# Performance work log

Hardware: AMD Instinct MI355X
Metric: run time of the kernel (lower is better)

## Reference

```python
import jax, jax.numpy as jnp
import numpy as np

B, S, D, H = 2, 2048, 2048, 16
HD = D // H


def setup_inputs() -> dict:
    key = jax.random.key(0)
    ks = jax.random.split(key, 9)
    scale = 0.02
    return {
        "x": jax.random.normal(ks[0], (B, S, D), dtype=jnp.float32),
        "wq_w": jax.random.normal(ks[1], (D, D), dtype=jnp.float32) * scale,
        "wq_b": jnp.zeros((D,), dtype=jnp.float32),
        "wk_w": jax.random.normal(ks[2], (D, D), dtype=jnp.float32) * scale,
        "wk_b": jnp.zeros((D,), dtype=jnp.float32),
        "wv_w": jax.random.normal(ks[3], (D, D), dtype=jnp.float32) * scale,
        "wv_b": jnp.zeros((D,), dtype=jnp.float32),
        "wo_w": jax.random.normal(ks[4], (D, D), dtype=jnp.float32) * scale,
        "wo_b": jnp.zeros((D,), dtype=jnp.float32),
    }


def reference(x, wq_w, wq_b, wk_w, wk_b, wv_w, wv_b, wo_w, wo_b):
    # torch Linear: y = x @ W.T + b
    q = x @ wq_w.T + wq_b  # [B,S,D]
    k = x @ wk_w.T + wk_b
    v = x @ wv_w.T + wv_b
    # [B,S,D] -> [B,H,S,HD]
    q = q.reshape(B, S, H, HD).transpose(0, 2, 1, 3)
    k = k.reshape(B, S, H, HD).transpose(0, 2, 1, 3)
    v = v.reshape(B, S, H, HD).transpose(0, 2, 1, 3)
    # scores [B,H,S,S], scaled by sqrt(d_dim) as in the original (not head_dim)
    scores = jnp.einsum("bhid,bhjd->bhij", q, k) / np.float32(np.sqrt(D))
    # faithful reproduction of the module's triu/transpose masking:
    m = jnp.swapaxes(jnp.triu(scores), -2, -1)  # lower-tri, zeros elsewhere
    p = jax.nn.softmax(m, axis=-2)              # softmax over dim=-2, zeros included
    a = jnp.swapaxes(jnp.triu(p), -2, -1)       # [B,H,S,S]
    attn = jnp.einsum("bhij,bhjd->bhid", a, v)  # [B,H,S,HD]
    concat = attn.transpose(0, 2, 1, 3).reshape(B, S, D)
    return concat @ wo_w.T + wo_b
```

## Files before the change

kernel.cpp:

```cpp
#include <hip/hip_runtime.h>

#define BB 2
#define SS 2048
#define DD 2048
#define HH 16
#define HDIM 128
#define MTOK (BB*SS)
#define BHH (BB*HH)
#define NCHUNK 16
#define QKN (2*DD)

typedef __attribute__((ext_vector_type(8))) __bf16 bf16x8;
typedef __attribute__((ext_vector_type(4))) float f32x4;
typedef __attribute__((ext_vector_type(8))) int i32x8;
typedef __attribute__((ext_vector_type(4))) int i32x4;

__device__ __forceinline__ unsigned short f2bf(float f) {
  unsigned u = __float_as_uint(f);
  u += 0x7FFFu + ((u >> 16) & 1u);
  return (unsigned short)(u >> 16);
}
__device__ __forceinline__ float bf2f(unsigned short s) {
  return __uint_as_float(((unsigned)s) << 16);
}
__device__ __forceinline__ unsigned char f2e4m3(float f) {
  int pk = __builtin_amdgcn_cvt_pk_fp8_f32(f, f, 0, false);
  return (unsigned char)(pk & 0xFF);
}

#define GLOAD_LDS16(src, dst)                                                   \
  __builtin_amdgcn_global_load_lds(                                             \
      (const void __attribute__((address_space(1)))*)(src),                     \
      (void __attribute__((address_space(3)))*)(dst), 16, 0, 0)

__device__ __forceinline__ void barrier_raw() {
  asm volatile("" ::: "memory");
  __builtin_amdgcn_s_barrier();
  asm volatile("" ::: "memory");
}

__global__ void cvt_x_dual(const float* __restrict__ in,
                           unsigned short* __restrict__ outb,
                           unsigned int* __restrict__ out8, int n4) {
  int i = blockIdx.x * blockDim.x + threadIdx.x;
  if (i < n4) {
    float4 v = ((const float4*)in)[i];
    ushort4 o;
    o.x = f2bf(v.x); o.y = f2bf(v.y); o.z = f2bf(v.z); o.w = f2bf(v.w);
    ((ushort4*)outb)[i] = o;
    int p0 = __builtin_amdgcn_cvt_pk_fp8_f32(v.x, v.y, 0, false);
    int p1 = __builtin_amdgcn_cvt_pk_fp8_f32(v.z, v.w, 0, false);
    out8[i] = (unsigned)(p0 & 0xFFFF) | ((unsigned)(p1 & 0xFFFF) << 16);
  }
}

__global__ void cvt_wqk8(const float* __restrict__ a, const float* __restrict__ b,
                         unsigned int* __restrict__ out) {
  int i = blockIdx.x * blockDim.x + threadIdx.x;
  int sel = i >> 20, r = i & 0xFFFFF;
  const float* src = sel == 0 ? a : b;
  float4 v = ((const float4*)src)[r];
  int p0 = __builtin_amdgcn_cvt_pk_fp8_f32(v.x, v.y, 0, false);
  int p1 = __builtin_amdgcn_cvt_pk_fp8_f32(v.z, v.w, 0, false);
  out[i] = (unsigned)(p0 & 0xFFFF) | ((unsigned)(p1 & 0xFFFF) << 16);
}

__global__ void cvt_w2bf(const float* __restrict__ a, const float* __restrict__ b,
                         unsigned short* __restrict__ out) {
  int i = blockIdx.x * blockDim.x + threadIdx.x;
  int sel = i >> 20, r = i & 0xFFFFF;
  const float* src = sel == 0 ? a : b;
  float4 v = ((const float4*)src)[r];
  ushort4 o;
  o.x = f2bf(v.x); o.y = f2bf(v.y); o.z = f2bf(v.z); o.w = f2bf(v.w);
  ((ushort4*)out)[i] = o;
}

__global__ void concat2(const float* __restrict__ a, const float* __restrict__ b,
                        float* __restrict__ out) {
  int i = blockIdx.x * blockDim.x + threadIdx.x;
  if (i < DD) { out[i] = a[i]; out[DD + i] = b[i]; }
}

template <bool OUT_BF16>
__global__ __launch_bounds__(512, 1) void gemm_bt8(
    const __bf16* __restrict__ A, const __bf16* __restrict__ W,
    const float* __restrict__ bias, void* __restrict__ Cout,
    int M, int N, int K) {
  __shared__ unsigned char lds[2][49152];
  const int t = threadIdx.x;
  const int lane = t & 63, wave = t >> 6;
  const int quad = lane >> 4, l16 = lane & 15;
  const int bid = blockIdx.x;
  const int swz = (bid & 7) * 32 + (bid >> 3);
  const int m0 = (swz >> 4) * 256;
  const int n0 = (swz & 15) * 128;
  const int wm = (wave >> 1) * 64;
  const int wn = (wave & 1) * 64;

  const __bf16* sA[4];
#pragma unroll
  for (int c = 0; c < 4; ++c) {
    int L = c * 512 + t;
    int row = L >> 3, p = L & 7;
    sA[c] = A + (size_t)(m0 + row) * K + ((p ^ (row & 7)) * 8);
  }
  const __bf16* sB[2];
#pragma unroll
  for (int c = 0; c < 2; ++c) {
    int L = c * 512 + t;
    int row = L >> 3, p = L & 7;
    sB[c] = W + (size_t)(n0 + row) * K + ((p ^ (row & 7)) * 8);
  }
  const int phk0 = (quad ^ (l16 & 7)) * 16;
  const int phk1 = ((4 + quad) ^ (l16 & 7)) * 16;

  f32x4 acc[4][4] = {};

  const int NT = K >> 6;

#pragma unroll
  for (int c = 0; c < 4; ++c)
    GLOAD_LDS16(sA[c], &lds[0][c * 8192 + wave * 1024]);
#pragma unroll
  for (int c = 0; c < 2; ++c)
    GLOAD_LDS16(sB[c], &lds[0][32768 + c * 8192 + wave * 1024]);

  for (int tt = 0; tt < NT; ++tt) {
    const int cur = tt & 1;
    const bool pf = (tt + 1 < NT);
    const int k1 = (tt + 1) << 6;

    if (pf) {
#pragma unroll
      for (int c = 0; c < 4; ++c)
        GLOAD_LDS16(sA[c] + k1, &lds[cur ^ 1][c * 8192 + wave * 1024]);
      asm volatile("s_waitcnt vmcnt(4)" ::: "memory");
    } else {
      asm volatile("s_waitcnt vmcnt(0)" ::: "memory");
    }
    barrier_raw();
    {
      bf16x8 af[4], bfv[4];
#pragma unroll
      for (int mt = 0; mt < 4; ++mt)
        af[mt] = *(const bf16x8*)&lds[cur][(wm + mt * 16 + l16) * 128 + phk0];
#pragma unroll
      for (int nt = 0; nt < 4; ++nt)
        bfv[nt] = *(const bf16x8*)&lds[cur][32768 + (wn + nt * 16 + l16) * 128 + phk0];
      __builtin_amdgcn_s_setprio(1);
#pragma unroll
      for (int mt = 0; mt < 4; ++mt)
#pragma unroll
        for (int nt = 0; nt < 4; ++nt)
          acc[mt][nt] = __builtin_amdgcn_mfma_f32_16x16x32_bf16(
              af[mt], bfv[nt], acc[mt][nt], 0, 0, 0);
      __builtin_amdgcn_s_setprio(0);
    }

    if (pf) {
#pragma unroll
      for (int c = 0; c < 2; ++c)
        GLOAD_LDS16(sB[c] + k1, &lds[cur ^ 1][32768 + c * 8192 + wave * 1024]);
    }
    barrier_raw();
    {
      bf16x8 af[4], bfv[4];
#pragma unroll
      for (int mt = 0; mt < 4; ++mt)
        af[mt] = *(const bf16x8*)&lds[cur][(wm + mt * 16 + l16) * 128 + phk1];
#pragma unroll
      for (int nt = 0; nt < 4; ++nt)
        bfv[nt] = *(const bf16x8*)&lds[cur][32768 + (wn + nt * 16 + l16) * 128 + phk1];
      __builtin_amdgcn_s_setprio(1);
#pragma unroll
      for (int mt = 0; mt < 4; ++mt)
#pragma unroll
        for (int nt = 0; nt < 4; ++nt)
          acc[mt][nt] = __builtin_amdgcn_mfma_f32_16x16x32_bf16(
              af[mt], bfv[nt], acc[mt][nt], 0, 0, 0);
      __builtin_amdgcn_s_setprio(0);
    }
    barrier_raw();
  }

#pragma unroll
  for (int mt = 0; mt < 4; ++mt) {
#pragma unroll
    for (int nt = 0; nt < 4; ++nt) {
      int col = n0 + wn + nt * 16 + l16;
      float bv = bias[col];
#pragma unroll
      for (int r = 0; r < 4; ++r) {
        int row = m0 + wm + mt * 16 + quad * 4 + r;
        float v = acc[mt][nt][r] + bv;
        if constexpr (OUT_BF16)
          ((unsigned short*)Cout)[(size_t)row * N + col] = f2bf(v);
        else
          ((float*)Cout)[(size_t)row * N + col] = v;
      }
    }
  }
}

__global__ __launch_bounds__(256, 2) void gemm_qk_fp8(
    const unsigned char* __restrict__ A8, const unsigned char* __restrict__ W8,
    const float* __restrict__ bias, unsigned char* __restrict__ Cout,
    int M, int N, int K) {
  __shared__ unsigned char lA[128 * 128];
  __shared__ unsigned char lB[128 * 128];
  const int t = threadIdx.x;
  const int lane = t & 63, wave = t >> 6;
  const int quad = lane >> 4, l16 = lane & 15;
  const int m0 = blockIdx.y * 128, n0 = blockIdx.x * 128;
  const int wm = (wave & 1) * 64, wn = (wave >> 1) * 64;
  const int p0 = (2 * quad) ^ (l16 & 7);

  f32x4 acc[4][4] = {};

  for (int k0 = 0; k0 < K; k0 += 128) {
#pragma unroll
    for (int c = 0; c < 4; ++c) {
      int lin = c * 256 + t;
      int row = lin >> 3;
      int ch = lin & 7;
      int sch = ch ^ (row & 7);
      const unsigned char* srcA = A8 + (size_t)(m0 + row) * K + k0 + sch * 16;
      const unsigned char* srcB = W8 + (size_t)(n0 + row) * K + k0 + sch * 16;
      GLOAD_LDS16(srcA, &lA[(c * 256 + wave * 64) * 16]);
      GLOAD_LDS16(srcB, &lB[(c * 256 + wave * 64) * 16]);
    }
    __syncthreads();
    i32x8 af[4];
#pragma unroll
    for (int mt = 0; mt < 4; ++mt) {
      int ra = (wm + mt * 16 + l16) * 128 + p0 * 16;
      ((i32x4*)&af[mt])[0] = *(const i32x4*)&lA[ra];
      ((i32x4*)&af[mt])[1] = *(const i32x4*)&lA[ra ^ 16];
    }
#pragma unroll
    for (int nt = 0; nt < 4; ++nt) {
      int rb = (wn + nt * 16 + l16) * 128 + p0 * 16;
      i32x8 bfr;
      ((i32x4*)&bfr)[0] = *(const i32x4*)&lB[rb];
      ((i32x4*)&bfr)[1] = *(const i32x4*)&lB[rb ^ 16];
#pragma unroll
      for (int mt = 0; mt < 4; ++mt)
        acc[mt][nt] = __builtin_amdgcn_mfma_scale_f32_16x16x128_f8f6f4(
            af[mt], bfr, acc[mt][nt], 0 , 0 ,
            0, 127 , 0, 127 );
    }
    __syncthreads();
  }

#pragma unroll
  for (int mt = 0; mt < 4; ++mt) {
#pragma unroll
    for (int nt = 0; nt < 4; ++nt) {
      int col = n0 + wn + nt * 16 + l16;
      float bv = bias[col];
#pragma unroll
      for (int r = 0; r < 4; ++r) {
        int row = m0 + wm + mt * 16 + quad * 4 + r;
        Cout[(size_t)row * N + col] = f2e4m3(acc[mt][nt][r] + bv);
      }
    }
  }
}

__global__ __launch_bounds__(256, 4) void qk_rowsum8(
    const unsigned char* __restrict__ q8, const unsigned char* __restrict__ k8,
    float* __restrict__ denomA, float* __restrict__ denomB,
    float* __restrict__ diag) {
  __shared__ unsigned char lK[2][128 * 128];
  __shared__ float redS[4][64];
  __shared__ float redD[4][64];
  const int t = threadIdx.x;
  const int lane = t & 63, wave = t >> 6;
  const int quad = lane >> 4, l16 = lane & 15;
  const int bh = blockIdx.y;
  const int b = bh >> 4, h = bh & 15;
  const int pair = blockIdx.x >> 1;
  const int half = blockIdx.x & 1;
  const float C = 0.03187935771f;
  const f32x4 fz = {0.f, 0.f, 0.f, 0.f};

  int soff[4];
#pragma unroll
  for (int c = 0; c < 4; ++c) {
    int L = c * 256 + t;
    int row = L >> 3, p = L & 7;
    soff[c] = row * QKN + ((p ^ (row & 7)) * 16);
  }
  const int p0 = (2 * quad) ^ (l16 & 7);
  int bo[2];
#pragma unroll
  for (int nt = 0; nt < 2; ++nt)
    bo[nt] = (wave * 32 + nt * 16 + l16) * 128 + p0 * 16;

  const unsigned char* kbase = k8 + (size_t)(b * SS) * QKN + h * HDIM;

  for (int sub = 0; sub < 2; ++sub) {
    const int tile = (sub == 0) ? pair : 31 - pair;
    const int i0 = tile * 64;
    const int jbase = i0 & ~127;
    const int ntile = (SS - jbase) >> 7;

    i32x8 af[4];
    {
      const unsigned char* qbase =
          q8 + (size_t)(b * SS + i0 + l16) * QKN + h * HDIM + quad * 32;
#pragma unroll
      for (int mt = 0; mt < 4; ++mt)
        af[mt] = *(const i32x8*)(qbase + (size_t)(mt * 16) * QKN);
    }

    float rowacc[4][4] = {};

    int kidx = half;
    if (kidx < ntile) {
      {
        const unsigned char* src = kbase + (size_t)(jbase + kidx * 128) * QKN;
#pragma unroll
        for (int c = 0; c < 4; ++c)
          GLOAD_LDS16(src + soff[c], &lK[0][(c * 256 + wave * 64) * 16]);
      }
      asm volatile("s_waitcnt vmcnt(0)" ::: "memory");
      __syncthreads();
      int cur = 0;
      for (; kidx < ntile; kidx += 2, cur ^= 1) {
        if (kidx + 2 < ntile) {
          const unsigned char* src =
              kbase + (size_t)(jbase + (kidx + 2) * 128) * QKN;
#pragma unroll
          for (int c = 0; c < 4; ++c)
            GLOAD_LDS16(src + soff[c], &lK[cur ^ 1][(c * 256 + wave * 64) * 16]);
        }
        const unsigned char* lkc = lK[cur];
        const int j0 = jbase + kidx * 128;
        if (kidx == 0) {
          float dloc[4][4] = {};
#pragma unroll
          for (int nt = 0; nt < 2; ++nt) {
            i32x8 bf;
            ((i32x4*)&bf)[0] = *(const i32x4*)(lkc + bo[nt]);
            ((i32x4*)&bf)[1] = *(const i32x4*)(lkc + (bo[nt] ^ 16));
            f32x4 acc[4];
#pragma unroll
            for (int mt = 0; mt < 4; ++mt)
              acc[mt] = __builtin_amdgcn_mfma_scale_f32_16x16x128_f8f6f4(
                  af[mt], bf, fz, 0, 0, 0, 127, 0, 127);
            const int colg = j0 + wave * 32 + nt * 16 + l16;
#pragma unroll
            for (int mt = 0; mt < 4; ++mt)
#pragma unroll
              for (int r = 0; r < 4; ++r) {
                int rg = i0 + mt * 16 + quad * 4 + r;
                float e = (colg >= rg)
                              ? __builtin_amdgcn_exp2f(acc[mt][r] * C) : 0.f;
                rowacc[mt][r] += e;
                if (colg == rg) dloc[mt][r] = e;
              }
          }
#pragma unroll
          for (int mt = 0; mt < 4; ++mt)
#pragma unroll
            for (int r = 0; r < 4; ++r) {
              float d = dloc[mt][r];
#pragma unroll
              for (int off = 1; off < 16; off <<= 1) d += __shfl_xor(d, off, 64);
              if (l16 == 0) redD[wave][mt * 16 + quad * 4 + r] = d;
            }
        } else {
#pragma unroll
          for (int nt = 0; nt < 2; ++nt) {
            i32x8 bf;
            ((i32x4*)&bf)[0] = *(const i32x4*)(lkc + bo[nt]);
            ((i32x4*)&bf)[1] = *(const i32x4*)(lkc + (bo[nt] ^ 16));
            f32x4 acc[4];
#pragma unroll
            for (int mt = 0; mt < 4; ++mt)
              acc[mt] = __builtin_amdgcn_mfma_scale_f32_16x16x128_f8f6f4(
                  af[mt], bf, fz, 0, 0, 0, 127, 0, 127);
#pragma unroll
            for (int mt = 0; mt < 4; ++mt)
#pragma unroll
              for (int r = 0; r < 4; ++r)
                rowacc[mt][r] += __builtin_amdgcn_exp2f(acc[mt][r] * C);
          }
        }
        asm volatile("s_waitcnt vmcnt(0)" ::: "memory");
        __syncthreads();
      }
    }

    __syncthreads();
#pragma unroll
    for (int mt = 0; mt < 4; ++mt)
#pragma unroll
      for (int r = 0; r < 4; ++r) {
        float s = rowacc[mt][r];
#pragma unroll
        for (int off = 1; off < 16; off <<= 1) s += __shfl_xor(s, off, 64);
        if (l16 == 0) redS[wave][mt * 16 + quad * 4 + r] = s;
      }
    __syncthreads();
    if (t < 64) {
      const int rg = i0 + t;
      float s = redS[0][t] + redS[1][t] + redS[2][t] + redS[3][t];
      if (half == 0) {
        denomA[bh * SS + rg] = (float)rg + s;
        diag[bh * SS + rg] = redD[0][t] + redD[1][t] + redD[2][t] + redD[3][t];
      } else {
        denomB[bh * SS + rg] = s;
      }
    }
  }
}

__global__ void scan_pass1(const __bf16* __restrict__ v0,
                           float* __restrict__ csum) {
  int blk = blockIdx.x;
  int bh = blk >> 4, c = blk & 15;
  int b = bh >> 4, h = bh & 15;
  int t = threadIdx.x;
  int rs = t >> 4, dg = t & 15;
  const unsigned short* base = (const unsigned short*)v0 +
      (size_t)(b * SS + c * 128 + rs * 8) * DD + h * HDIM + dg * 8;
  float s[8] = {0.f, 0.f, 0.f, 0.f, 0.f, 0.f, 0.f, 0.f};
#pragma unroll
  for (int i = 0; i < 8; ++i) {
    uint4 u = *(const uint4*)(base + (size_t)i * DD);
    const unsigned short* us = (const unsigned short*)&u;
#pragma unroll
    for (int j = 0; j < 8; ++j) s[j] += bf2f(us[j]);
  }
  __shared__ float red[16 * 128];
#pragma unroll
  for (int j = 0; j < 8; ++j) red[rs * 128 + dg * 8 + j] = s[j];
  __syncthreads();
  for (int st = 8; st >= 1; st >>= 1) {
    if (rs < st) {
#pragma unroll
      for (int j = 0; j < 8; ++j)
        red[rs * 128 + dg * 8 + j] += red[(rs + st) * 128 + dg * 8 + j];
    }
    __syncthreads();
  }
  if (rs == 0) {
#pragma unroll
    for (int j = 0; j < 8; ++j)
      csum[(size_t)blk * 128 + dg * 8 + j] = red[dg * 8 + j];
  }
}

__global__ void scan_pass2(const __bf16* __restrict__ v0,
                           const float* __restrict__ csum,
                           const float* __restrict__ denomA,
                           const float* __restrict__ denomB,
                           const float* __restrict__ diag,
                           unsigned short* __restrict__ ctx) {
  int blk = blockIdx.x;
  int bh = blk >> 4, c = blk & 15;
  int b = bh >> 4, h = bh & 15;
  int t = threadIdx.x;
  int rs = t >> 4, dg = t & 15;
  const unsigned short* vbase = (const unsigned short*)v0 +
      (size_t)(b * SS + c * 128 + rs * 8) * DD + h * HDIM + dg * 8;
  float vrow[8][8];
  float ls[8] = {0.f, 0.f, 0.f, 0.f, 0.f, 0.f, 0.f, 0.f};
#pragma unroll
  for (int i = 0; i < 8; ++i) {
    uint4 u = *(const uint4*)(vbase + (size_t)i * DD);
    const unsigned short* us = (const unsigned short*)&u;
#pragma unroll
    for (int j = 0; j < 8; ++j) {
      vrow[i][j] = bf2f(us[j]);
      ls[j] += vrow[i][j];
    }
  }
  __shared__ float red[16 * 128];
#pragma unroll
  for (int j = 0; j < 8; ++j) red[rs * 128 + dg * 8 + j] = ls[j];
  __syncthreads();

  float pre[8] = {0.f, 0.f, 0.f, 0.f, 0.f, 0.f, 0.f, 0.f};
  for (int cc = 0; cc < c; ++cc) {
    const float* cp = csum + (size_t)(bh * 16 + cc) * 128 + dg * 8;
#pragma unroll
    for (int j = 0; j < 8; ++j) pre[j] += cp[j];
  }
  for (int ss2 = 0; ss2 < rs; ++ss2) {
#pragma unroll
    for (int j = 0; j < 8; ++j) pre[j] += red[ss2 * 128 + dg * 8 + j];
  }

  int row0 = c * 128 + rs * 8;
  unsigned short* obase =
      ctx + (size_t)(b * SS + row0) * DD + h * HDIM + dg * 8;
  const float* dnA = denomA + bh * SS + row0;
  const float* dnB = denomB + bh * SS + row0;
  const float* dgp = diag + bh * SS + row0;
#pragma unroll
  for (int i = 0; i < 8; ++i) {
    float inv = 1.0f / (dnA[i] + dnB[i]);
    float dv = dgp[i];
    unsigned short o[8];
#pragma unroll
    for (int j = 0; j < 8; ++j) {
      float val = (pre[j] + dv * vrow[i][j]) * inv;
      o[j] = f2bf(val);
      pre[j] += vrow[i][j];
    }
    *(uint4*)(obase + (size_t)i * DD) = *(const uint4*)o;
  }
}

extern "C" void kernel_launch(void* const* d_in, const int* in_sizes, int n_in,
                              void* d_out, int out_size, void* d_ws, size_t ws_size,
                              hipStream_t stream) {
  (void)in_sizes; (void)n_in; (void)out_size; (void)ws_size;
  const float* x    = (const float*)d_in[0];
  const float* wq_w = (const float*)d_in[1];
  const float* wq_b = (const float*)d_in[2];
  const float* wk_w = (const float*)d_in[3];
  const float* wk_b = (const float*)d_in[4];
  const float* wv_w = (const float*)d_in[5];
  const float* wv_b = (const float*)d_in[6];
  const float* wo_w = (const float*)d_in[7];
  const float* wo_b = (const float*)d_in[8];

  char* ws = (char*)d_ws;
  size_t off = 0;
  auto alloc = [&](size_t bytes) {
    char* p = ws + off;
    off += (bytes + 255) & ~(size_t)255;
    return p;
  };
  unsigned short* xb   = (unsigned short*)alloc((size_t)MTOK * DD * 2);
  unsigned char*  x8   = (unsigned char*)alloc((size_t)MTOK * DD);
  unsigned char*  wqk8 = (unsigned char*)alloc((size_t)2 * DD * DD);
  unsigned short* wvo  = (unsigned short*)alloc((size_t)2 * DD * DD * 2);
  unsigned char*  qk8  = (unsigned char*)alloc((size_t)MTOK * QKN);
  unsigned short* v    = (unsigned short*)alloc((size_t)MTOK * DD * 2);
  unsigned short* ctx  = (unsigned short*)alloc((size_t)MTOK * DD * 2);
  float* biasqk = (float*)alloc((size_t)2 * DD * 4);
  float* denomA = (float*)alloc((size_t)BHH * SS * 4);
  float* denomB = (float*)alloc((size_t)BHH * SS * 4);
  float* diag   = (float*)alloc((size_t)BHH * SS * 4);
  float* csum   = (float*)alloc((size_t)BHH * NCHUNK * 128 * 4);

  {
    int n4 = MTOK * DD / 4;
    cvt_x_dual<<<n4 / 256, 256, 0, stream>>>(x, xb, (unsigned int*)x8, n4);
    cvt_wqk8<<<(2 << 20) / 256, 256, 0, stream>>>(wq_w, wk_w, (unsigned int*)wqk8);
    cvt_w2bf<<<(2 << 20) / 256, 256, 0, stream>>>(wv_w, wo_w, wvo);
    concat2<<<(DD + 255) / 256, 256, 0, stream>>>(wq_b, wk_b, biasqk);
  }

  gemm_qk_fp8<<<dim3(QKN / 128, MTOK / 128), 256, 0, stream>>>(
      x8, wqk8, biasqk, qk8, MTOK, QKN, DD);

  gemm_bt8<true><<<(MTOK / 256) * (DD / 128), 512, 0, stream>>>(
      (const __bf16*)xb, (const __bf16*)wvo, wv_b, v, MTOK, DD, DD);

  qk_rowsum8<<<dim3(32, BHH), 256, 0, stream>>>(
      qk8,
      qk8 + DD,
      denomA, denomB, diag);

  scan_pass1<<<BHH * NCHUNK, 256, 0, stream>>>((const __bf16*)v, csum);
  scan_pass2<<<BHH * NCHUNK, 256, 0, stream>>>((const __bf16*)v, csum,
                                               denomA, denomB, diag, ctx);

  gemm_bt8<false><<<(MTOK / 256) * (DD / 128), 512, 0, stream>>>(
      (const __bf16*)ctx, (const __bf16*)(wvo + (size_t)DD * DD), wo_b,
      d_out, MTOK, DD, DD);
}
```

Before: 316.7 us.

## Double-buffer FP8 QK GEMM with 256x128 tiles, split B prefetch, and block swizzle

Rewrites the FP8 Q/K projection GEMM to use 512-thread blocks with 256x128 output tiles and double-buffered LDS. The next k-tile's A and B loads are issued while MFMAs run on the current buffer, with the B prefetch split between two half-compute phases. A block-index swizzle is added for L2 locality, and s_setprio raises priority around the MFMA bursts. The goal is to hide global-load latency that the old load-sync-compute-sync loop exposed, at the cost of 96KB LDS and one block per CU.

```diff
diff --git a/kernel.cpp b/kernel.cpp
--- a/kernel.cpp
+++ b/kernel.cpp
@@ -203,54 +203,111 @@
   }
 }
 
-__global__ __launch_bounds__(256, 2) void gemm_qk_fp8(
+__global__ __launch_bounds__(512, 1) void gemm_qk8(
     const unsigned char* __restrict__ A8, const unsigned char* __restrict__ W8,
     const float* __restrict__ bias, unsigned char* __restrict__ Cout,
     int M, int N, int K) {
-  __shared__ unsigned char lA[128 * 128];
-  __shared__ unsigned char lB[128 * 128];
+  __shared__ unsigned char lds[2][49152];
   const int t = threadIdx.x;
   const int lane = t & 63, wave = t >> 6;
   const int quad = lane >> 4, l16 = lane & 15;
-  const int m0 = blockIdx.y * 128, n0 = blockIdx.x * 128;
-  const int wm = (wave & 1) * 64, wn = (wave >> 1) * 64;
+  const int bid = blockIdx.x;
+  const int swz = (bid & 7) * 64 + (bid >> 3);
+  const int m0 = (swz >> 5) * 256;
+  const int n0 = (swz & 31) * 128;
+  const int wm = (wave >> 1) * 64;
+  const int wn = (wave & 1) * 64;
+
+  const unsigned char* sA[4];
+#pragma unroll
+  for (int c = 0; c < 4; ++c) {
+    int L = c * 512 + t;
+    int row = L >> 3, p = L & 7;
+    sA[c] = A8 + (size_t)(m0 + row) * K + ((p ^ (row & 7)) * 16);
+  }
+  const unsigned char* sB[2];
+#pragma unroll
+  for (int c = 0; c < 2; ++c) {
+    int L = c * 512 + t;
+    int row = L >> 3, p = L & 7;
+    sB[c] = W8 + (size_t)(n0 + row) * K + ((p ^ (row & 7)) * 16);
+  }
   const int p0 = (2 * quad) ^ (l16 & 7);
 
   f32x4 acc[4][4] = {};
 
-  for (int k0 = 0; k0 < K; k0 += 128) {
-#pragma unroll
-    for (int c = 0; c < 4; ++c) {
-      int lin = c * 256 + t;
-      int row = lin >> 3;
-      int ch = lin & 7;
-      int sch = ch ^ (row & 7);
-      const unsigned char* srcA = A8 + (size_t)(m0 + row) * K + k0 + sch * 16;
-      const unsigned char* srcB = W8 + (size_t)(n0 + row) * K + k0 + sch * 16;
-      GLOAD_LDS16(srcA, &lA[(c * 256 + wave * 64) * 16]);
-      GLOAD_LDS16(srcB, &lB[(c * 256 + wave * 64) * 16]);
-    }
-    __syncthreads();
+  const int NT = K >> 7;
+
+#pragma unroll
+  for (int c = 0; c < 4; ++c)
+    GLOAD_LDS16(sA[c], &lds[0][c * 8192 + wave * 1024]);
+#pragma unroll
+  for (int c = 0; c < 2; ++c)
+    GLOAD_LDS16(sB[c], &lds[0][32768 + c * 8192 + wave * 1024]);
+
+  for (int tt = 0; tt < NT; ++tt) {
+    const int cur = tt & 1;
+    const bool pf = (tt + 1 < NT);
+    const int k1 = (tt + 1) << 7;
+
+    if (pf) {
+#pragma unroll
+      for (int c = 0; c < 4; ++c)
+        GLOAD_LDS16(sA[c] + k1, &lds[cur ^ 1][c * 8192 + wave * 1024]);
+      asm volatile("s_waitcnt vmcnt(4)" ::: "memory");
+    } else {
+      asm volatile("s_waitcnt vmcnt(0)" ::: "memory");
+    }
+    barrier_raw();
     i32x8 af[4];
-#pragma unroll
-    for (int mt = 0; mt < 4; ++mt) {
-      int ra = (wm + mt * 16 + l16) * 128 + p0 * 16;
-      ((i32x4*)&af[mt])[0] = *(const i32x4*)&lA[ra];
-      ((i32x4*)&af[mt])[1] = *(const i32x4*)&lA[ra ^ 16];
-    }
-#pragma unroll
-    for (int nt = 0; nt < 4; ++nt) {
-      int rb = (wn + nt * 16 + l16) * 128 + p0 * 16;
-      i32x8 bfr;
-      ((i32x4*)&bfr)[0] = *(const i32x4*)&lB[rb];
-      ((i32x4*)&bfr)[1] = *(const i32x4*)&lB[rb ^ 16];
+    {
+#pragma unroll
+      for (int mt = 0; mt < 4; ++mt) {
+        int ra = (wm + mt * 16 + l16) * 128 + p0 * 16;
+        ((i32x4*)&af[mt])[0] = *(const i32x4*)&lds[cur][ra];
+        ((i32x4*)&af[mt])[1] = *(const i32x4*)&lds[cur][ra ^ 16];
+      }
+      i32x8 bv[2];
+#pragma unroll
+      for (int nt = 0; nt < 2; ++nt) {
+        int rb = 32768 + (wn + nt * 16 + l16) * 128 + p0 * 16;
+        ((i32x4*)&bv[nt])[0] = *(const i32x4*)&lds[cur][rb];
+        ((i32x4*)&bv[nt])[1] = *(const i32x4*)&lds[cur][rb ^ 16];
+      }
+      __builtin_amdgcn_s_setprio(1);
 #pragma unroll
       for (int mt = 0; mt < 4; ++mt)
-        acc[mt][nt] = __builtin_amdgcn_mfma_scale_f32_16x16x128_f8f6f4(
-            af[mt], bfr, acc[mt][nt], 0 , 0 ,
-            0, 127 , 0, 127 );
-    }
-    __syncthreads();
+#pragma unroll
+        for (int nt = 0; nt < 2; ++nt)
+          acc[mt][nt] = __builtin_amdgcn_mfma_scale_f32_16x16x128_f8f6f4(
+              af[mt], bv[nt], acc[mt][nt], 0, 0, 0, 127, 0, 127);
+      __builtin_amdgcn_s_setprio(0);
+    }
+
+    if (pf) {
+#pragma unroll
+      for (int c = 0; c < 2; ++c)
+        GLOAD_LDS16(sB[c] + k1, &lds[cur ^ 1][32768 + c * 8192 + wave * 1024]);
+    }
+    barrier_raw();
+    {
+      i32x8 bv[2];
+#pragma unroll
+      for (int nt = 0; nt < 2; ++nt) {
+        int rb = 32768 + (wn + (nt + 2) * 16 + l16) * 128 + p0 * 16;
+        ((i32x4*)&bv[nt])[0] = *(const i32x4*)&lds[cur][rb];
+        ((i32x4*)&bv[nt])[1] = *(const i32x4*)&lds[cur][rb ^ 16];
+      }
+      __builtin_amdgcn_s_setprio(1);
+#pragma unroll
+      for (int mt = 0; mt < 4; ++mt)
+#pragma unroll
+        for (int nt = 0; nt < 2; ++nt)
+          acc[mt][nt + 2] = __builtin_amdgcn_mfma_scale_f32_16x16x128_f8f6f4(
+              af[mt], bv[nt], acc[mt][nt + 2], 0, 0, 0, 127, 0, 127);
+      __builtin_amdgcn_s_setprio(0);
+    }
+    barrier_raw();
   }
 
 #pragma unroll
@@ -558,7 +615,7 @@
     concat2<<<(DD + 255) / 256, 256, 0, stream>>>(wq_b, wk_b, biasqk);
   }
 
-  gemm_qk_fp8<<<dim3(QKN / 128, MTOK / 128), 256, 0, stream>>>(
+  gemm_qk8<<<(MTOK / 256) * (QKN / 128), 512, 0, stream>>>(
       x8, wqk8, biasqk, qk8, MTOK, QKN, DD);
 
   gemm_bt8<true><<<(MTOK / 256) * (DD / 128), 512, 0, stream>>>(
```

Measured after the change: 320.9 us. About the same (+1.3%).
